# Optimization experiments

Measured on AMD Instinct MI355X. Metric: run time of the kernel, lower is better.

The kernel has to match this reference:

```python
import jax, jax.numpy as jnp
import numpy as np

N_E = 1024
E_DIM = 64
BETA = 0.4
N_TOK = 131072


def setup_inputs() -> dict:
    key = jax.random.key(0)
    k1, k2 = jax.random.split(key)
    z = jax.random.normal(k1, (N_TOK, E_DIM), dtype=jnp.float32)
    # torch init: uniform(-1/n_e, 1/n_e)
    codebook = jax.random.uniform(k2, (N_E, E_DIM), dtype=jnp.float32,
                                  minval=-1.0 / N_E, maxval=1.0 / N_E)
    return {"z": z, "codebook": codebook}


def reference(z, codebook):
    sg = jax.lax.stop_gradient
    # squared euclidean distances: [N, n_e]
    d = (jnp.sum(z * z, axis=1, keepdims=True)
         + jnp.sum(codebook * codebook, axis=1)
         - 2.0 * jnp.matmul(z, codebook.T))
    idx = jnp.argmin(d, axis=1)                      # [N]
    z_q = codebook[idx]                              # gather, [N, E_DIM]
    # commitment / codebook loss
    vq_loss = (jnp.mean((sg(z_q) - z) ** 2)
               + BETA * jnp.mean((z_q - sg(z)) ** 2))
    # straight-through estimator
    z_q_st = z + sg(z_q - z)
    # codebook usage statistics (mean of one-hot encodings)
    e_mean = jnp.bincount(idx, length=N_E).astype(z.dtype) / jnp.asarray(idx.shape[0], z.dtype)
    usage_loss = -jnp.sum(e_mean * jnp.log(e_mean + 1e-10))
    perplexity = jnp.exp(usage_loss)
    vq_loss = vq_loss + 0.01 * usage_loss
    return z_q_st, vq_loss, idx[:, None], perplexity
```

## Files before the change

### kernel.cpp

```cpp
#include <hip/hip_runtime.h>
#include <math.h>

#define N_TOK 131072
#define N_E   1024
#define E_DIM 64
#define BETA  0.4

#define ZQ_OFF   0
#define LOSS_OFF 8388608
#define IDX_OFF  8388609
#define PERP_OFF 8519681

#define WS_C2    0
#define WS_CNT   4096
#define WS_SSQ   8192
#define WS_WLC   8200
#define WS_FHI   8208
#define WS_FLO   139280
#define WS_WL    270352
#define WS_Z2    303120
#define WS_KEYS  335888
#define WLCAP    8192

typedef short bf16x8 __attribute__((ext_vector_type(8)));
typedef float f32x4  __attribute__((ext_vector_type(4)));
typedef unsigned long long u64;

__device__ __forceinline__ unsigned short f32_to_bf16_rn(float f) {
    unsigned u = __float_as_uint(f);
    unsigned r = (u + 0x7fffu + ((u >> 16) & 1u)) >> 16;
    return (unsigned short)r;
}
__device__ __forceinline__ float bf16_to_f32(unsigned short h) {
    return __uint_as_float(((unsigned)h) << 16);
}
__device__ __forceinline__ void gl2lds16(const void* g, void* l) {
    __builtin_amdgcn_global_load_lds(
        (const __attribute__((address_space(1))) unsigned int*)g,
        (__attribute__((address_space(3))) unsigned int*)l, 16, 0, 0);
}

__global__ void c2_kernel(const float* __restrict__ cb, float* __restrict__ c2) {
    int e = blockIdx.x * blockDim.x + threadIdx.x;
    if (e < N_E) {
        const float* p = cb + (size_t)e * E_DIM;
        double s = 0.0;
#pragma unroll
        for (int k = 0; k < E_DIM; ++k) {
            double c = (double)p[k];
            s = fma(c, c, s);
        }
        c2[e] = (float)s;
    }
}

__global__ void frag_kernel(const float* __restrict__ cb,
                            unsigned short* __restrict__ fhi,
                            unsigned short* __restrict__ flo) {
    int tid = blockIdx.x * 256 + threadIdx.x;
    int j  = tid & 7;
    int l  = (tid >> 3) & 63;
    int cc = tid >> 9;
    int code = (cc >> 1) * 16 + (l & 15);
    int k    = (cc & 1) * 32 + (l >> 4) * 8 + j;
    float f = cb[(size_t)code * E_DIM + k];
    unsigned short h = f32_to_bf16_rn(f);
    unsigned short lo = f32_to_bf16_rn(f - bf16_to_f32(h));
    fhi[tid] = h;
    flo[tid] = lo;
}

__device__ __attribute__((noinline)) int exact_best_serial(
    const float* __restrict__ z, const float* __restrict__ cb,
    const float* __restrict__ c2, int n) {
    const float* zr = z + (size_t)n * E_DIM;
    float r[8];
#pragma unroll
    for (int j = 0; j < 8; ++j) r[j] = __fmul_rn(zr[j], zr[j]);
#pragma unroll 1
    for (int i = 8; i < 64; i += 8)
#pragma unroll
        for (int j = 0; j < 8; ++j)
            r[j] = __fadd_rn(r[j], __fmul_rn(zr[i + j], zr[i + j]));
    float z2 = __fadd_rn(__fadd_rn(__fadd_rn(r[0], r[1]), __fadd_rn(r[2], r[3])),
                         __fadd_rn(__fadd_rn(r[4], r[5]), __fadd_rn(r[6], r[7])));
    u64 bestkey = ~0ull;
#pragma unroll 1
    for (int e = 0; e < N_E; ++e) {
        const float* cp = cb + (size_t)e * E_DIM;
        double m = 0.0;
#pragma unroll 1
        for (int i = 0; i < E_DIM; ++i)
            m = fma((double)zr[i], (double)cp[i], m);
        float d = __fsub_rn(__fadd_rn(z2, c2[e]), __fmul_rn(2.0f, (float)m));
        u64 key = ((u64)__float_as_uint(d) << 32) | (unsigned)e;
        if (key < bestkey) bestkey = key;
    }
    return (int)(bestkey & 0xffffffffu);
}

__global__ __launch_bounds__(256, 4) void vq_main(
    const float* __restrict__ z, const float* __restrict__ cb,
    const float* __restrict__ c2, const unsigned short* __restrict__ fhi_,
    const unsigned short* __restrict__ flo_, int* __restrict__ counts,
    double* __restrict__ sum_sq, int* __restrict__ wl_count,
    int* __restrict__ wl, float margin, float* __restrict__ out) {

    __shared__ unsigned char stagebuf[2][16384];
    __shared__ float c2s[N_E];
    __shared__ int   best_s[128];
    __shared__ unsigned char flag_s[128];
    __shared__ double wred[4];

    const int tid  = threadIdx.x;
    const int lane = tid & 63;
    const int wid  = tid >> 6;
    const int col  = lane & 15;
    const int quad = lane >> 4;
    const int blk_tok0 = blockIdx.x * 128;
    const int wave_tok0 = blk_tok0 + wid * 32;

#pragma unroll
    for (int i = 0; i < 4; ++i) c2s[tid * 4 + i] = c2[tid * 4 + i] + 0.5f;

    bf16x8 Ah[2][2], Al[2][2];
#pragma unroll
    for (int m = 0; m < 2; ++m) {
        const float* zr = z + (size_t)(wave_tok0 + m * 16 + col) * E_DIM + quad * 8;
#pragma unroll
        for (int kc = 0; kc < 2; ++kc) {
            float4 u0 = *(const float4*)(zr + kc * 32);
            float4 u1 = *(const float4*)(zr + kc * 32 + 4);
            float f[8] = {u0.x, u0.y, u0.z, u0.w, u1.x, u1.y, u1.z, u1.w};
            union { unsigned short u[8]; bf16x8 v; } h, lo;
#pragma unroll
            for (int j = 0; j < 8; ++j) {
                h.u[j]  = f32_to_bf16_rn(f[j]);
                lo.u[j] = f32_to_bf16_rn(f[j] - bf16_to_f32(h.u[j]));
            }
            Ah[m][kc] = h.v;
            Al[m][kc] = lo.v;
        }
    }

    unsigned k1[2][4], k2[2][4];
#pragma unroll
    for (int m = 0; m < 2; ++m)
#pragma unroll
        for (int r = 0; r < 4; ++r) { k1[m][r] = 0xFFFFFFFFu; k2[m][r] = 0xFFFFFFFFu; }

    const char* hsrc0 = (const char*)fhi_;
    const char* lsrc0 = (const char*)flo_;
    auto stage = [&](int s, int b) {
#pragma unroll
        for (int i = 0; i < 2; ++i) {
            gl2lds16(hsrc0 + s * 8192 + i * 4096 + tid * 16,
                     &stagebuf[b][i * 4096 + wid * 1024]);
            gl2lds16(lsrc0 + s * 8192 + i * 4096 + tid * 16,
                     &stagebuf[b][8192 + i * 4096 + wid * 1024]);
        }
    };

    stage(0, 0);
    for (int s = 0; s < 16; ++s) {
        __syncthreads();
        if (s + 1 < 16) stage(s + 1, (s + 1) & 1);
        const unsigned char* hb = &stagebuf[s & 1][0];
        const unsigned char* lb = &stagebuf[s & 1][8192];
#pragma unroll
        for (int cl = 0; cl < 4; ++cl) {
            const int c = s * 4 + cl;
            const int off0 = (cl * 2) * 1024 + lane * 16;
            union { uint4 u; bf16x8 v; } bh0, bh1, bl0, bl1;
            bh0.u = *(const uint4*)(hb + off0);
            bh1.u = *(const uint4*)(hb + off0 + 1024);
            bl0.u = *(const uint4*)(lb + off0);
            bl1.u = *(const uint4*)(lb + off0 + 1024);
            const float c2p5 = c2s[c * 16 + col];
#pragma unroll
            for (int m = 0; m < 2; ++m) {
                f32x4 acc1 = {0.f, 0.f, 0.f, 0.f};
                f32x4 acc2 = {0.f, 0.f, 0.f, 0.f};
                acc1 = __builtin_amdgcn_mfma_f32_16x16x32_bf16(Ah[m][0], bh0.v, acc1, 0, 0, 0);
                acc2 = __builtin_amdgcn_mfma_f32_16x16x32_bf16(Ah[m][0], bl0.v, acc2, 0, 0, 0);
                acc1 = __builtin_amdgcn_mfma_f32_16x16x32_bf16(Ah[m][1], bh1.v, acc1, 0, 0, 0);
                acc2 = __builtin_amdgcn_mfma_f32_16x16x32_bf16(Ah[m][1], bl1.v, acc2, 0, 0, 0);
                acc1 = __builtin_amdgcn_mfma_f32_16x16x32_bf16(Al[m][0], bh0.v, acc1, 0, 0, 0);
                acc1 = __builtin_amdgcn_mfma_f32_16x16x32_bf16(Al[m][1], bh1.v, acc1, 0, 0, 0);
#pragma unroll
                for (int r = 0; r < 4; ++r) {
                    float t = fmaf(-2.f, acc1[r], fmaf(-2.f, acc2[r], c2p5));
                    unsigned key = (__float_as_uint(t) & 0xFFFFFFC0u) | (unsigned)c;
                    unsigned lo2 = max(k1[m][r], key);
                    k2[m][r] = min(k2[m][r], lo2);
                    k1[m][r] = min(k1[m][r], key);
                }
            }
        }
        __syncthreads();
    }

#pragma unroll
    for (int m = 0; m < 2; ++m) {
#pragma unroll
        for (int r = 0; r < 4; ++r) {
            float v1 = __uint_as_float(k1[m][r] & 0xFFFFFFC0u);
            float v2 = __uint_as_float(k2[m][r] & 0xFFFFFFC0u);
            int   b1 = (int)(k1[m][r] & 63u) * 16 + col;
#pragma unroll
            for (int d = 1; d < 16; d <<= 1) {
                float o1 = __shfl_xor(v1, d, 64);
                float o2 = __shfl_xor(v2, d, 64);
                int   ob = __shfl_xor(b1, d, 64);
                float n2 = fminf(fminf(v2, o2), fmaxf(v1, o1));
                bool take = (o1 < v1) || (o1 == v1 && ob < b1);
                v1 = fminf(v1, o1);
                b1 = take ? ob : b1;
                v2 = n2;
            }
            if (col == 0) {
                int tl = wid * 32 + m * 16 + quad * 4 + r;
                int n  = blk_tok0 + tl;
                int best = b1;
                bool fl = (v2 - v1) < margin;
                if (fl) {
                    int pos = atomicAdd(wl_count, 1);
                    if (pos < WLCAP) wl[pos] = n;
                    else { best = exact_best_serial(z, cb, c2, n); fl = false; }
                }
                best_s[tl] = best;
                flag_s[tl] = fl ? 1 : 0;
                if (!fl) {
                    out[IDX_OFF + n] = (float)best;
                    atomicAdd(&counts[best], 1);
                }
            }
        }
    }
    __syncthreads();

    const int sub = tid & 15, grp = tid >> 4;
    double dl = 0.0;
    const float4* zrow = (const float4*)z;
    const float4* crow = (const float4*)cb;
    float4* qrow = (float4*)(out + ZQ_OFF);
#pragma unroll
    for (int p = 0; p < 8; ++p) {
        int tl = p * 16 + grp;
        if (!flag_s[tl]) {
            int n = blk_tok0 + tl;
            float4 z4 = zrow[(size_t)n * 16 + sub];
            float4 c4 = crow[(size_t)best_s[tl] * 16 + sub];
            float dx = c4.x - z4.x, dy = c4.y - z4.y;
            float dz = c4.z - z4.z, dw = c4.w - z4.w;
            float4 q;
            q.x = z4.x + dx; q.y = z4.y + dy;
            q.z = z4.z + dz; q.w = z4.w + dw;
            qrow[(size_t)n * 16 + sub] = q;
            dl += (double)dx * dx + (double)dy * dy
                + (double)dz * dz + (double)dw * dw;
        }
    }
#pragma unroll
    for (int off = 32; off > 0; off >>= 1)
        dl += __shfl_down(dl, off, 64);
    if (lane == 0) wred[wid] = dl;
    __syncthreads();
    if (tid == 0)
        atomicAdd(sum_sq, wred[0] + wred[1] + wred[2] + wred[3]);
}

__global__ __launch_bounds__(256) void z2_kernel(
    const float* __restrict__ z, const int* __restrict__ wl,
    const int* __restrict__ wl_count, float* __restrict__ z2arr) {
    int idx = blockIdx.x * 256 + threadIdx.x;
    int count = *wl_count; if (count > WLCAP) count = WLCAP;
    if (idx >= count) return;
    const float* zr = z + (size_t)wl[idx] * E_DIM;
    float r[8];
#pragma unroll
    for (int j = 0; j < 8; ++j) r[j] = __fmul_rn(zr[j], zr[j]);
#pragma unroll
    for (int i = 8; i < 64; i += 8)
#pragma unroll
        for (int j = 0; j < 8; ++j)
            r[j] = __fadd_rn(r[j], __fmul_rn(zr[i + j], zr[i + j]));
    z2arr[idx] = __fadd_rn(
        __fadd_rn(__fadd_rn(r[0], r[1]), __fadd_rn(r[2], r[3])),
        __fadd_rn(__fadd_rn(r[4], r[5]), __fadd_rn(r[6], r[7])));
}

__global__ __launch_bounds__(64) void fixup_scan(
    const float* __restrict__ z, const float* __restrict__ cb,
    const float* __restrict__ c2, const int* __restrict__ wl,
    const int* __restrict__ wl_count, const float* __restrict__ z2arr,
    u64* __restrict__ keys) {

    int count = *wl_count; if (count > WLCAP) count = WLCAP;
    const int g = blockIdx.x >> 5;
    const int s = blockIdx.x & 31;
    if (g * 64 >= count) return;
    const int lane = threadIdx.x;
    const int w = g * 64 + lane;
    const bool valid = w < count;
    const int n = wl[valid ? w : g * 64];

    double zd[E_DIM];
    const float4* zp = (const float4*)(z + (size_t)n * E_DIM);
#pragma unroll
    for (int k = 0; k < 16; ++k) {
        float4 v = zp[k];
        zd[4 * k]     = (double)v.x;
        zd[4 * k + 1] = (double)v.y;
        zd[4 * k + 2] = (double)v.z;
        zd[4 * k + 3] = (double)v.w;
    }
    const float z2 = valid ? z2arr[w] : 0.f;

    u64 best = ~0ull;
    const int e0 = s * 32;
    for (int e = e0; e < e0 + 32; ++e) {
        const float* cp = cb + (size_t)e * E_DIM;
        double m = 0.0;
#pragma unroll
        for (int i = 0; i < E_DIM; ++i)
            m = fma(zd[i], (double)cp[i], m);
        float d = __fsub_rn(__fadd_rn(z2, c2[e]), __fmul_rn(2.0f, (float)m));
        u64 key = ((u64)__float_as_uint(d) << 32) | (unsigned)e;
        if (key < best) best = key;
    }
    if (valid) atomicMin(&keys[w], best);
}

__global__ __launch_bounds__(256) void fixup_apply(
    const float* __restrict__ z, const float* __restrict__ cb,
    const int* __restrict__ wl, const int* __restrict__ wl_count,
    const u64* __restrict__ keys, int* __restrict__ counts,
    double* __restrict__ sum_sq, float* __restrict__ out) {

    int count = *wl_count; if (count > WLCAP) count = WLCAP;
    const int lane = threadIdx.x & 63;
    const int gw = blockIdx.x * 4 + (threadIdx.x >> 6);
    for (int w = gw; w < count; w += 1024) {
        const int n = wl[w];
        const int best = (int)(keys[w] & 0xffffffffull);
        float cv = cb[(size_t)best * E_DIM + lane];
        float zi = z[(size_t)n * E_DIM + lane];
        float diff = cv - zi;
        out[ZQ_OFF + (size_t)n * E_DIM + lane] = zi + diff;
        double d2 = (double)diff * (double)diff;
#pragma unroll
        for (int off = 32; off > 0; off >>= 1)
            d2 += __shfl_down(d2, off, 64);
        if (lane == 0) {
            atomicAdd(sum_sq, d2);
            atomicAdd(&counts[best], 1);
            out[IDX_OFF + n] = (float)best;
        }
    }
}

__global__ __launch_bounds__(1024) void finalize_kernel(
    const int* __restrict__ counts, const double* __restrict__ sum_sq,
    float* __restrict__ out) {
    __shared__ double red[1024];
    int e = threadIdx.x;
    double em = (double)counts[e] / (double)N_TOK;
    red[e] = -em * log(em + 1e-10);
    __syncthreads();
    for (int s = 512; s > 0; s >>= 1) {
        if (e < s) red[e] += red[e + s];
        __syncthreads();
    }
    if (e == 0) {
        double usage = red[0];
        double mse = sum_sq[0] / (double)((size_t)N_TOK * E_DIM);
        out[LOSS_OFF] = (float)((1.0 + BETA) * mse + 0.01 * usage);
        out[PERP_OFF] = (float)exp(usage);
    }
}

extern "C" void kernel_launch(void* const* d_in, const int* in_sizes, int n_in,
                              void* d_out, int out_size, void* d_ws, size_t ws_size,
                              hipStream_t stream) {
    const float* z  = (const float*)d_in[0];
    const float* cb = (const float*)d_in[1];
    float* out = (float*)d_out;

    float*          c2     = (float*)((char*)d_ws + WS_C2);
    int*            counts = (int*)((char*)d_ws + WS_CNT);
    double*         sum_sq = (double*)((char*)d_ws + WS_SSQ);
    int*            wlc    = (int*)((char*)d_ws + WS_WLC);
    unsigned short* fhi    = (unsigned short*)((char*)d_ws + WS_FHI);
    unsigned short* flo    = (unsigned short*)((char*)d_ws + WS_FLO);
    int*            wl     = (int*)((char*)d_ws + WS_WL);
    float*          z2arr  = (float*)((char*)d_ws + WS_Z2);
    u64*            keys   = (u64*)((char*)d_ws + WS_KEYS);

    float margin = (ws_size >= (size_t)(WS_KEYS + 8 * WLCAP)) ? 4.5e-5f : 0.0f;

    hipMemsetAsync((char*)d_ws + WS_CNT, 0, WS_FHI - WS_CNT, stream);
    hipMemsetAsync((char*)d_ws + WS_KEYS, 0xFF, 8 * WLCAP, stream);

    c2_kernel<<<4, 256, 0, stream>>>(cb, c2);
    frag_kernel<<<256, 256, 0, stream>>>(cb, fhi, flo);
    vq_main<<<1024, 256, 0, stream>>>(z, cb, c2, fhi, flo, counts, sum_sq,
                                      wlc, wl, margin, out);
    z2_kernel<<<32, 256, 0, stream>>>(z, wl, wlc, z2arr);
    fixup_scan<<<4096, 64, 0, stream>>>(z, cb, c2, wl, wlc, z2arr, keys);
    fixup_apply<<<256, 256, 0, stream>>>(z, cb, wl, wlc, keys, counts,
                                         sum_sq, out);
    finalize_kernel<<<1, 1024, 0, stream>>>(counts, sum_sq, out);
}
```

Before: 226.5 us.

## Fold workspace memsets into prep kernels, fuse z2 into fixup, seed MFMA with codebook norm

Removes the two hipMemsetAsync calls by zeroing counters in c2_kernel and initialising fixup keys in frag_kernel. Drops the separate z2_kernel and recomputes the squared norm inside fixup_scan. In vq_main the codebook-norm term is folded into the MFMA accumulator init, the search is flipped to a max over a scaled score with reversed tags, the MFMA chains are split into two independent accumulators, and the trailing barrier per stage is removed. Index output is written coalesced from shared memory. This cuts launch count and per-element ALU work, but dropping the second barrier relies on the next iteration's leading barrier to protect the double buffer.

New measurement: 218.0 us. -3.8%, faster.

```diff
diff --git a/kernel.cpp b/kernel.cpp
--- a/kernel.cpp
+++ b/kernel.cpp
@@ -18,8 +18,7 @@
 #define WS_FHI   8208
 #define WS_FLO   139280
 #define WS_WL    270352
-#define WS_Z2    303120
-#define WS_KEYS  335888
+#define WS_KEYS  303120
 #define WLCAP    8192
 
 typedef short bf16x8 __attribute__((ext_vector_type(8)));
@@ -40,7 +39,9 @@
         (__attribute__((address_space(3))) unsigned int*)l, 16, 0, 0);
 }
 
-__global__ void c2_kernel(const float* __restrict__ cb, float* __restrict__ c2) {
+__global__ void c2_kernel(const float* __restrict__ cb, float* __restrict__ c2,
+                          int* __restrict__ counts, int* __restrict__ wlc,
+                          double* __restrict__ sum_sq) {
     int e = blockIdx.x * blockDim.x + threadIdx.x;
     if (e < N_E) {
         const float* p = cb + (size_t)e * E_DIM;
@@ -51,13 +52,17 @@
             s = fma(c, c, s);
         }
         c2[e] = (float)s;
+        counts[e] = 0;
+        if (e == 0) { *wlc = 0; *sum_sq = 0.0; }
     }
 }
 
 __global__ void frag_kernel(const float* __restrict__ cb,
                             unsigned short* __restrict__ fhi,
-                            unsigned short* __restrict__ flo) {
+                            unsigned short* __restrict__ flo,
+                            u64* __restrict__ keys) {
     int tid = blockIdx.x * 256 + threadIdx.x;
+    if (tid < WLCAP) keys[tid] = ~0ull;
     int j  = tid & 7;
     int l  = (tid >> 3) & 63;
     int cc = tid >> 9;
@@ -104,7 +109,7 @@
     const float* __restrict__ c2, const unsigned short* __restrict__ fhi_,
     const unsigned short* __restrict__ flo_, int* __restrict__ counts,
     double* __restrict__ sum_sq, int* __restrict__ wl_count,
-    int* __restrict__ wl, float margin, float* __restrict__ out) {
+    int* __restrict__ wl, float margin_u, float* __restrict__ out) {
 
     __shared__ unsigned char stagebuf[2][16384];
     __shared__ float c2s[N_E];
@@ -121,7 +126,8 @@
     const int wave_tok0 = blk_tok0 + wid * 32;
 
 #pragma unroll
-    for (int i = 0; i < 4; ++i) c2s[tid * 4 + i] = c2[tid * 4 + i] + 0.5f;
+    for (int i = 0; i < 4; ++i)
+        c2s[tid * 4 + i] = fmaf(-0.5f, c2[tid * 4 + i], 0.25f);
 
     bf16x8 Ah[2][2], Al[2][2];
 #pragma unroll
@@ -147,7 +153,7 @@
 #pragma unroll
     for (int m = 0; m < 2; ++m)
 #pragma unroll
-        for (int r = 0; r < 4; ++r) { k1[m][r] = 0xFFFFFFFFu; k2[m][r] = 0xFFFFFFFFu; }
+        for (int r = 0; r < 4; ++r) { k1[m][r] = 0u; k2[m][r] = 0u; }
 
     const char* hsrc0 = (const char*)fhi_;
     const char* lsrc0 = (const char*)flo_;
@@ -161,6 +167,7 @@
         }
     };
 
+    const f32x4 zero4 = {0.f, 0.f, 0.f, 0.f};
     stage(0, 0);
     for (int s = 0; s < 16; ++s) {
         __syncthreads();
@@ -176,28 +183,27 @@
             bh1.u = *(const uint4*)(hb + off0 + 1024);
             bl0.u = *(const uint4*)(lb + off0);
             bl1.u = *(const uint4*)(lb + off0 + 1024);
-            const float c2p5 = c2s[c * 16 + col];
+            const float ch = c2s[c * 16 + col];
+            const f32x4 cinit = {ch, ch, ch, ch};
+            const unsigned ctag = (unsigned)(63 - c);
 #pragma unroll
             for (int m = 0; m < 2; ++m) {
-                f32x4 acc1 = {0.f, 0.f, 0.f, 0.f};
-                f32x4 acc2 = {0.f, 0.f, 0.f, 0.f};
-                acc1 = __builtin_amdgcn_mfma_f32_16x16x32_bf16(Ah[m][0], bh0.v, acc1, 0, 0, 0);
-                acc2 = __builtin_amdgcn_mfma_f32_16x16x32_bf16(Ah[m][0], bl0.v, acc2, 0, 0, 0);
-                acc1 = __builtin_amdgcn_mfma_f32_16x16x32_bf16(Ah[m][1], bh1.v, acc1, 0, 0, 0);
+                f32x4 acc1 = __builtin_amdgcn_mfma_f32_16x16x32_bf16(Ah[m][0], bh0.v, cinit, 0, 0, 0);
+                f32x4 acc2 = __builtin_amdgcn_mfma_f32_16x16x32_bf16(Ah[m][1], bh1.v, zero4, 0, 0, 0);
+                acc1 = __builtin_amdgcn_mfma_f32_16x16x32_bf16(Ah[m][0], bl0.v, acc1, 0, 0, 0);
                 acc2 = __builtin_amdgcn_mfma_f32_16x16x32_bf16(Ah[m][1], bl1.v, acc2, 0, 0, 0);
                 acc1 = __builtin_amdgcn_mfma_f32_16x16x32_bf16(Al[m][0], bh0.v, acc1, 0, 0, 0);
-                acc1 = __builtin_amdgcn_mfma_f32_16x16x32_bf16(Al[m][1], bh1.v, acc1, 0, 0, 0);
+                acc2 = __builtin_amdgcn_mfma_f32_16x16x32_bf16(Al[m][1], bh1.v, acc2, 0, 0, 0);
 #pragma unroll
                 for (int r = 0; r < 4; ++r) {
-                    float t = fmaf(-2.f, acc1[r], fmaf(-2.f, acc2[r], c2p5));
-                    unsigned key = (__float_as_uint(t) & 0xFFFFFFC0u) | (unsigned)c;
-                    unsigned lo2 = max(k1[m][r], key);
-                    k2[m][r] = min(k2[m][r], lo2);
-                    k1[m][r] = min(k1[m][r], key);
+                    float u = acc1[r] + acc2[r];
+                    unsigned key = (__float_as_uint(u) & 0xFFFFFFC0u) | ctag;
+                    unsigned hi2 = min(k1[m][r], key);
+                    k2[m][r] = max(k2[m][r], hi2);
+                    k1[m][r] = max(k1[m][r], key);
                 }
             }
         }
-        __syncthreads();
     }
 
 #pragma unroll
@@ -206,15 +212,15 @@
         for (int r = 0; r < 4; ++r) {
             float v1 = __uint_as_float(k1[m][r] & 0xFFFFFFC0u);
             float v2 = __uint_as_float(k2[m][r] & 0xFFFFFFC0u);
-            int   b1 = (int)(k1[m][r] & 63u) * 16 + col;
+            int   b1 = (63 - (int)(k1[m][r] & 63u)) * 16 + col;
 #pragma unroll
             for (int d = 1; d < 16; d <<= 1) {
                 float o1 = __shfl_xor(v1, d, 64);
                 float o2 = __shfl_xor(v2, d, 64);
                 int   ob = __shfl_xor(b1, d, 64);
-                float n2 = fminf(fminf(v2, o2), fmaxf(v1, o1));
-                bool take = (o1 < v1) || (o1 == v1 && ob < b1);
-                v1 = fminf(v1, o1);
+                float n2 = fmaxf(fmaxf(v2, o2), fminf(v1, o1));
+                bool take = (o1 > v1) || (o1 == v1 && ob < b1);
+                v1 = fmaxf(v1, o1);
                 b1 = take ? ob : b1;
                 v2 = n2;
             }
@@ -222,7 +228,7 @@
                 int tl = wid * 32 + m * 16 + quad * 4 + r;
                 int n  = blk_tok0 + tl;
                 int best = b1;
-                bool fl = (v2 - v1) < margin;
+                bool fl = (v1 - v2) < margin_u;
                 if (fl) {
                     int pos = atomicAdd(wl_count, 1);
                     if (pos < WLCAP) wl[pos] = n;
@@ -230,14 +236,13 @@
                 }
                 best_s[tl] = best;
                 flag_s[tl] = fl ? 1 : 0;
-                if (!fl) {
-                    out[IDX_OFF + n] = (float)best;
-                    atomicAdd(&counts[best], 1);
-                }
+                if (!fl) atomicAdd(&counts[best], 1);
             }
         }
     }
     __syncthreads();
+
+    if (tid < 128) out[IDX_OFF + blk_tok0 + tid] = (float)best_s[tid];
 
     const int sub = tid & 15, grp = tid >> 4;
     double dl = 0.0;
@@ -270,31 +275,10 @@
         atomicAdd(sum_sq, wred[0] + wred[1] + wred[2] + wred[3]);
 }
 
-__global__ __launch_bounds__(256) void z2_kernel(
-    const float* __restrict__ z, const int* __restrict__ wl,
-    const int* __restrict__ wl_count, float* __restrict__ z2arr) {
-    int idx = blockIdx.x * 256 + threadIdx.x;
-    int count = *wl_count; if (count > WLCAP) count = WLCAP;
-    if (idx >= count) return;
-    const float* zr = z + (size_t)wl[idx] * E_DIM;
-    float r[8];
-#pragma unroll
-    for (int j = 0; j < 8; ++j) r[j] = __fmul_rn(zr[j], zr[j]);
-#pragma unroll
-    for (int i = 8; i < 64; i += 8)
-#pragma unroll
-        for (int j = 0; j < 8; ++j)
-            r[j] = __fadd_rn(r[j], __fmul_rn(zr[i + j], zr[i + j]));
-    z2arr[idx] = __fadd_rn(
-        __fadd_rn(__fadd_rn(r[0], r[1]), __fadd_rn(r[2], r[3])),
-        __fadd_rn(__fadd_rn(r[4], r[5]), __fadd_rn(r[6], r[7])));
-}
-
 __global__ __launch_bounds__(64) void fixup_scan(
     const float* __restrict__ z, const float* __restrict__ cb,
     const float* __restrict__ c2, const int* __restrict__ wl,
-    const int* __restrict__ wl_count, const float* __restrict__ z2arr,
-    u64* __restrict__ keys) {
+    const int* __restrict__ wl_count, u64* __restrict__ keys) {
 
     int count = *wl_count; if (count > WLCAP) count = WLCAP;
     const int g = blockIdx.x >> 5;
@@ -315,7 +299,22 @@
         zd[4 * k + 2] = (double)v.z;
         zd[4 * k + 3] = (double)v.w;
     }
-    const float z2 = valid ? z2arr[w] : 0.f;
+    float r8[8];
+#pragma unroll
+    for (int j = 0; j < 8; ++j) {
+        float f = (float)zd[j];
+        r8[j] = __fmul_rn(f, f);
+    }
+#pragma unroll
+    for (int i = 8; i < 64; i += 8)
+#pragma unroll
+        for (int j = 0; j < 8; ++j) {
+            float f = (float)zd[i + j];
+            r8[j] = __fadd_rn(r8[j], __fmul_rn(f, f));
+        }
+    const float z2 = __fadd_rn(
+        __fadd_rn(__fadd_rn(r8[0], r8[1]), __fadd_rn(r8[2], r8[3])),
+        __fadd_rn(__fadd_rn(r8[4], r8[5]), __fadd_rn(r8[6], r8[7])));
 
     u64 best = ~0ull;
     const int e0 = s * 32;
@@ -394,20 +393,15 @@
     unsigned short* fhi    = (unsigned short*)((char*)d_ws + WS_FHI);
     unsigned short* flo    = (unsigned short*)((char*)d_ws + WS_FLO);
     int*            wl     = (int*)((char*)d_ws + WS_WL);
-    float*          z2arr  = (float*)((char*)d_ws + WS_Z2);
     u64*            keys   = (u64*)((char*)d_ws + WS_KEYS);
 
-    float margin = (ws_size >= (size_t)(WS_KEYS + 8 * WLCAP)) ? 4.5e-5f : 0.0f;
-
-    hipMemsetAsync((char*)d_ws + WS_CNT, 0, WS_FHI - WS_CNT, stream);
-    hipMemsetAsync((char*)d_ws + WS_KEYS, 0xFF, 8 * WLCAP, stream);
-
-    c2_kernel<<<4, 256, 0, stream>>>(cb, c2);
-    frag_kernel<<<256, 256, 0, stream>>>(cb, fhi, flo);
+    float margin_u = (ws_size >= (size_t)(WS_KEYS + 8 * WLCAP)) ? 2.25e-5f : 0.0f;
+
+    c2_kernel<<<4, 256, 0, stream>>>(cb, c2, counts, wlc, sum_sq);
+    frag_kernel<<<256, 256, 0, stream>>>(cb, fhi, flo, keys);
     vq_main<<<1024, 256, 0, stream>>>(z, cb, c2, fhi, flo, counts, sum_sq,
-                                      wlc, wl, margin, out);
-    z2_kernel<<<32, 256, 0, stream>>>(z, wl, wlc, z2arr);
-    fixup_scan<<<4096, 64, 0, stream>>>(z, cb, c2, wl, wlc, z2arr, keys);
+                                      wlc, wl, margin_u, out);
+    fixup_scan<<<4096, 64, 0, stream>>>(z, cb, c2, wl, wlc, keys);
     fixup_apply<<<256, 256, 0, stream>>>(z, cb, wl, wlc, keys, counts,
                                          sum_sq, out);
     finalize_kernel<<<1, 1024, 0, stream>>>(counts, sum_sq, out);
```
